# Performance work log

Hardware: AMD Instinct MI355X
Metric: run time of the kernel (lower is better)

The kernel has to match this reference:

```python
import jax, jax.numpy as jnp
import numpy as np

VOCAB, EMB, FEAT = 30000, 300, 2048
B, NQ, NW, NK = 256, 32, 12, 64


def setup_inputs() -> dict:
    key = jax.random.key(0)
    ks = jax.random.split(key, 10)
    return {
        "wv": jax.random.normal(ks[0], (VOCAB, EMB), jnp.float32),
        "Wf": jax.random.normal(ks[1], (EMB, FEAT), jnp.float32) * 0.02,
        "bf": jax.random.normal(ks[2], (EMB,), jnp.float32) * 0.02,
        "Wp": jax.random.normal(ks[3], (EMB, EMB), jnp.float32) * 0.05,
        "bp": jax.random.normal(ks[4], (EMB,), jnp.float32) * 0.02,
        "Wm": jax.random.normal(ks[5], (EMB, EMB), jnp.float32) * 0.05,
        "bm": jax.random.normal(ks[6], (EMB,), jnp.float32) * 0.02,
        "feature": jax.random.normal(ks[7], (B, NK, FEAT), jnp.float32),
        "query": jax.random.randint(ks[8], (B, NQ, NW), 0, VOCAB),
        "label": jax.random.randint(ks[9], (B, NK), 0, VOCAB),
    }


def reference(wv, Wf, bf, Wp, bp, Wm, bm, feature, query, label):
    # Dropouts act as identity in eval mode.
    eps = 1e-5
    q_emb = wv[query]                                   # [B, queries, words, D]
    k_emb = wv[label] + feature @ Wf.T + bf             # [B, objects, D]
    scale = 1.0 / np.sqrt(EMB)
    att = jnp.einsum('byqd,bkd->byqk', q_emb, k_emb) * scale
    att = jax.nn.softmax(att, axis=-1)                  # over objects
    q_max_att = jnp.max(att, axis=3)                    # [B, queries, words]
    neg_inf = -jnp.finfo(q_max_att.dtype).max
    q_max_att = jnp.where(query == 0, neg_inf, q_max_att)
    q_max_norm_att = jax.nn.softmax(q_max_att, axis=-1) / 5.0
    p_emb = jnp.einsum('byq,byqd->byd', q_max_norm_att, q_emb)  # [B, queries, D]
    p_emb = (p_emb @ Wp.T + bp) + eps * (p_emb @ Wm.T + bm)
    return p_emb, k_emb
```

## Files before the change

kernel.cpp:

```cpp
#include <hip/hip_runtime.h>

typedef unsigned short u16;
typedef unsigned int u32;
typedef __bf16 bf16x8 __attribute__((ext_vector_type(8)));
typedef float f32x4 __attribute__((ext_vector_type(4)));

#if defined(__has_builtin)
#  if __has_builtin(__builtin_amdgcn_cvt_pk_bf16_f32)
#    define PK_BF16 1
#  endif
#endif

__device__ __forceinline__ u16 f2bu(float f){
  u32 u = __float_as_uint(f);
  return (u16)((u + 0x7fffu + ((u >> 16) & 1u)) >> 16);
}
__device__ __forceinline__ float b2f(u16 u){
  union { float f; u32 i; } v; v.i = ((u32)u) << 16; return v.f;
}
__device__ __forceinline__ u32 pkbf(float a, float b){
#ifdef PK_BF16
  typedef __bf16 bf16x2 __attribute__((ext_vector_type(2)));
  union { bf16x2 h; u32 u; } c;
  c.h = __builtin_amdgcn_cvt_pk_bf16_f32(a, b);
  return c.u;
#else
  return (u32)f2bu(a) | ((u32)f2bu(b) << 16);
#endif
}
__device__ __forceinline__ void glds16(const u16* g, u16* l){
  __builtin_amdgcn_global_load_lds(
      (const __attribute__((address_space(1))) void*)g,
      (__attribute__((address_space(3))) void*)l, 16, 0, 0);
}
__device__ __forceinline__ void glds16f(const float* g, float* l){
  __builtin_amdgcn_global_load_lds(
      (const __attribute__((address_space(1))) void*)g,
      (__attribute__((address_space(3))) void*)l, 16, 0, 0);
}

__global__ __launch_bounds__(256) void prep_wc(
    const float* __restrict__ Wp, const float* __restrict__ bp,
    const float* __restrict__ Wm, const float* __restrict__ bm,
    u16* __restrict__ Wc, float* __restrict__ bc)
{
  int idx = blockIdx.x * 256 + threadIdx.x;
  if (idx < 384 * 160) {
    int n = idx / 160, k = (idx % 160) * 2;
    float v0 = 0.f, v1 = 0.f;
    if (n < 300 && k < 300) {
      v0 = Wp[n * 300 + k]     + 1e-5f * Wm[n * 300 + k];
      v1 = Wp[n * 300 + k + 1] + 1e-5f * Wm[n * 300 + k + 1];
    }
    ((u32*)Wc)[idx] = pkbf(v0, v1);
    if (idx < 384) bc[idx] = (idx < 300) ? bp[idx] + 1e-5f * bm[idx] : 0.f;
  }
}

__global__ __launch_bounds__(256) void prep_wv16(
    const float* __restrict__ wv, u16* __restrict__ wv16)
{
  int idx = blockIdx.x * 256 + threadIdx.x;
  if (idx < 30000 * 160) {
    int row = idx / 160, k = (idx % 160) * 2;
    float v0 = 0.f, v1 = 0.f;
    if (k < 300) {
      v0 = wv[(size_t)row * 300 + k];
      v1 = wv[(size_t)row * 300 + k + 1];
    }
    ((u32*)wv16)[idx] = pkbf(v0, v1);
  }
}

__global__ __launch_bounds__(256) void prep_wf16(
    const float* __restrict__ Wf, u16* __restrict__ Wf16)
{
  int i = blockIdx.x * 256 + threadIdx.x;
  if (i < 384 * 1024) {
    int row = i >> 10, c2 = (i & 1023) * 2;
    float v0 = 0.f, v1 = 0.f;
    if (row < 300) {
      v0 = Wf[(size_t)row * 2048 + c2];
      v1 = Wf[(size_t)row * 2048 + c2 + 1];
    }
    ((u32*)Wf16)[i] = pkbf(v0, v1);
  }
}

template <int GLDS>
__global__ __launch_bounds__(256) void gemm0_kernel(
    const float* __restrict__ A, const float* __restrict__ B,
    const u16* __restrict__ Af16, const u16* __restrict__ Bf16,
    const float* __restrict__ bias,
    const int* __restrict__ label, const float* __restrict__ wv,
    float* __restrict__ C, u16* __restrict__ kemb16)
{
  __shared__ __align__(16) u16 As[128 * 32];
  __shared__ __align__(16) u16 Bs[128 * 32];
  const int lda = 2048, K = 2048, nbn = 3, nsrc = 300;
  int t = threadIdx.x;
  int bm = (blockIdx.x / nbn) * 128;
  int bn = (blockIdx.x % nbn) * 128;
  int lane = t & 63, w = t >> 6;
  int wm = (w >> 1) * 64, wn = (w & 1) * 64;

  f32x4 acc[4][4];
  for (int i = 0; i < 4; i++)
    for (int j = 0; j < 4; j++)
      for (int r = 0; r < 4; r++) acc[i][j][r] = 0.f;

  int mrow = lane & 15, q = lane >> 4;

  for (int kk = 0; kk < K; kk += 32) {
    #pragma unroll
    for (int p = 0; p < 2; p++) {
      int idx = t + p * 256;
      int row = idx >> 2, ch = idx & 3;
      int brow = bn + row;
      if (brow >= nsrc) brow = 0;
      const float4* ap = (const float4*)&A[(size_t)(bm + row) * lda + kk + ch * 8];
      float4 a0 = ap[0], a1 = ap[1];
      const float4* bpp = (const float4*)&B[(size_t)brow * lda + kk + ch * 8];
      float4 b0 = bpp[0], b1 = bpp[1];
      union { u32 u[4]; uint4 v; } pa, pb;
      pa.u[0] = pkbf(a0.x, a0.y); pa.u[1] = pkbf(a0.z, a0.w);
      pa.u[2] = pkbf(a1.x, a1.y); pa.u[3] = pkbf(a1.z, a1.w);
      pb.u[0] = pkbf(b0.x, b0.y); pb.u[1] = pkbf(b0.z, b0.w);
      pb.u[2] = pkbf(b1.x, b1.y); pb.u[3] = pkbf(b1.z, b1.w);
      *(uint4*)&As[idx * 8] = pa.v;
      *(uint4*)&Bs[idx * 8] = pb.v;
    }
    __syncthreads();

    bf16x8 af[4], bfr[4];
    #pragma unroll
    for (int i = 0; i < 4; i++)
      af[i] = *(const bf16x8*)&As[(wm + i * 16 + mrow) * 32 + q * 8];
    #pragma unroll
    for (int j = 0; j < 4; j++)
      bfr[j] = *(const bf16x8*)&Bs[(wn + j * 16 + mrow) * 32 + q * 8];
    #pragma unroll
    for (int i = 0; i < 4; i++)
      #pragma unroll
      for (int j = 0; j < 4; j++)
        acc[i][j] = __builtin_amdgcn_mfma_f32_16x16x32_bf16(
            af[i], bfr[j], acc[i][j], 0, 0, 0);
    __syncthreads();
  }

  #pragma unroll
  for (int i = 0; i < 4; i++)
    #pragma unroll
    for (int j = 0; j < 4; j++) {
      int col = bn + wn + j * 16 + (lane & 15);
      int rb = bm + wm + i * 16 + (lane >> 4) * 4;
      #pragma unroll
      for (int r = 0; r < 4; r++) {
        int m = rb + r;
        if (col < 300) {
          float v = acc[i][j][r];
          v += bias[col] + wv[(size_t)label[m] * 300 + col];
          C[(size_t)m * 300 + col] = v;
          if (kemb16) kemb16[(size_t)m * 320 + col] = f2bu(v);
        } else if (kemb16 && col < 320) {
          kemb16[(size_t)m * 320 + col] = 0;
        }
      }
    }
}

__global__ __launch_bounds__(256) void gemm0v6_kernel(
    const float* __restrict__ A, const u16* __restrict__ Bf16,
    float* __restrict__ P3)
{
  __shared__ __align__(16) float As[128 * 32];
  __shared__ __align__(16) u16  Bs[128 * 32];
  int t = threadIdx.x;
  int lane = t & 63, w = t >> 6;
  int g = blockIdx.x;
  int xcd = g & 7, seq = g >> 3;
  int mloc = seq / 9, rem = seq % 9;
  int nn = rem % 3, kc = rem / 3;
  int bm = (xcd * 16 + mloc) * 128;
  int bn = nn * 128;
  int k0 = kc * 672, kend = (kc == 2) ? 2048 : k0 + 672;
  int wm = (w >> 1) * 64, wn = (w & 1) * 64;
  int mrow = lane & 15, q = lane >> 4;

  f32x4 acc[4][4];
  #pragma unroll
  for (int i = 0; i < 4; i++)
    #pragma unroll
    for (int j = 0; j < 4; j++)
      #pragma unroll
      for (int r = 0; r < 4; r++) acc[i][j][r] = 0.f;

  int rlA = lane >> 3, chA = lane & 7;
  int rlB = lane >> 2, chB = lane & 3;
  const float* gA = &A[(size_t)(bm + w * 32 + rlA) * 2048 + ((chA ^ rlA) << 2)];
  const u16*   gB = &Bf16[(size_t)(bn + w * 32 + rlB) * 2048 + (chB << 3)];
  float* lA = &As[(w * 32) * 32];
  u16*   lB = &Bs[(w * 32) * 32];

  for (int kk = k0; kk < kend; kk += 32) {
    #pragma unroll
    for (int p = 0; p < 4; p++)
      glds16f(gA + (size_t)p * 8 * 2048 + kk, lA + p * 8 * 32);
    #pragma unroll
    for (int p = 0; p < 2; p++)
      glds16(gB + (size_t)p * 16 * 2048 + kk, lB + p * 16 * 32);
    __syncthreads();

    bf16x8 af[4], bfr[4];
    #pragma unroll
    for (int i = 0; i < 4; i++) {
      int r = wm + i * 16 + mrow;
      int c0 = ((2 * q) ^ (r & 7)) * 4;
      int c1 = ((2 * q + 1) ^ (r & 7)) * 4;
      f32x4 x = *(const f32x4*)&As[r * 32 + c0];
      f32x4 y = *(const f32x4*)&As[r * 32 + c1];
      union { u32 u[4]; bf16x8 h; } cc;
      cc.u[0] = pkbf(x[0], x[1]); cc.u[1] = pkbf(x[2], x[3]);
      cc.u[2] = pkbf(y[0], y[1]); cc.u[3] = pkbf(y[2], y[3]);
      af[i] = cc.h;
    }
    #pragma unroll
    for (int j = 0; j < 4; j++)
      bfr[j] = *(const bf16x8*)&Bs[(wn + j * 16 + mrow) * 32 + q * 8];
    #pragma unroll
    for (int i = 0; i < 4; i++)
      #pragma unroll
      for (int j = 0; j < 4; j++)
        acc[i][j] = __builtin_amdgcn_mfma_f32_16x16x32_bf16(
            af[i], bfr[j], acc[i][j], 0, 0, 0);
    __syncthreads();
  }

  #pragma unroll
  for (int i = 0; i < 4; i++)
    #pragma unroll
    for (int j = 0; j < 4; j++) {
      int col = bn + wn + j * 16 + (lane & 15);
      if (col >= 300) continue;
      int rb = bm + wm + i * 16 + (lane >> 4) * 4;
      #pragma unroll
      for (int r = 0; r < 4; r++)
        P3[(size_t)kc * 4915200 + (size_t)(rb + r) * 300 + col] = acc[i][j][r];
    }
}

__global__ __launch_bounds__(256) void reduce_kernel(
    const float* __restrict__ P3, const float* __restrict__ bf,
    const int* __restrict__ label, const float* __restrict__ wv,
    float* __restrict__ C, u16* __restrict__ kemb16)
{
  int idx = blockIdx.x * 256 + threadIdx.x;
  if (idx >= 16384 * 80) return;
  int m = idx / 80, c4 = idx % 80;
  if (c4 < 75) {
    int c = c4 * 4;
    float4 a = *(const float4*)&P3[(size_t)m * 300 + c];
    float4 b = *(const float4*)&P3[(size_t)4915200 + (size_t)m * 300 + c];
    float4 d = *(const float4*)&P3[(size_t)9830400 + (size_t)m * 300 + c];
    float4 wvv = *(const float4*)&wv[(size_t)label[m] * 300 + c];
    float4 bfv = *(const float4*)&bf[c];
    float4 v;
    v.x = a.x + b.x + d.x + bfv.x + wvv.x;
    v.y = a.y + b.y + d.y + bfv.y + wvv.y;
    v.z = a.z + b.z + d.z + bfv.z + wvv.z;
    v.w = a.w + b.w + d.w + bfv.w + wvv.w;
    *(float4*)&C[(size_t)m * 300 + c] = v;
    union { u16 h[4]; uint2 u; } o;
    o.h[0] = f2bu(v.x); o.h[1] = f2bu(v.y);
    o.h[2] = f2bu(v.z); o.h[3] = f2bu(v.w);
    *(uint2*)&kemb16[(size_t)m * 320 + c] = o.u;
  } else {
    int c = 300 + (c4 - 75) * 4;
    uint2 z; z.x = 0; z.y = 0;
    *(uint2*)&kemb16[(size_t)m * 320 + c] = z;
  }
}

#define KES 344
template <int FULL>
__global__ __launch_bounds__(256) void attn_kernel(
    const float* __restrict__ wv, const u16* __restrict__ wv16,
    const int* __restrict__ query,
    const float* __restrict__ kout, const u16* __restrict__ kemb16,
    u16* __restrict__ praw)
{
  __shared__ __align__(16) u16 ke[64 * KES];
  __shared__ __align__(16) int qoff[192];
  __shared__ __align__(16) float awd[192];
  __shared__ __align__(16) float wt[192];

  int blk = blockIdx.x, b = blk >> 1, bh = blk & 1;
  int t = threadIdx.x;
  int lane = t & 63, w = t >> 6;

  if (FULL) {
    for (int i = t; i < 2560; i += 256) {
      int row = i / 40, ch = i % 40;
      *(uint4*)&ke[row * KES + ch * 8] =
          *(const uint4*)&kemb16[(size_t)(b * 64 + row) * 320 + ch * 8];
    }
  } else {
    for (int i = t; i < 4800; i += 256) {
      int row = i / 75, c4 = i % 75;
      float4 v = *(const float4*)&kout[(size_t)(b * 64 + row) * 300 + c4 * 4];
      *(u32*)&ke[row * KES + c4 * 4]     = pkbf(v.x, v.y);
      *(u32*)&ke[row * KES + c4 * 4 + 2] = pkbf(v.z, v.w);
    }
    for (int i = t; i < 640; i += 256) {
      int row = i / 10, c2 = i % 10;
      *(u32*)&ke[row * KES + 300 + c2 * 2] = 0;
    }
  }
  if (t < 192)
    qoff[t] = query[b * 384 + bh * 192 + t] * (FULL ? 320 : 300);
  __syncthreads();

  int mrow = lane & 15, q = lane >> 4;
  f32x4 acc[3][4];
  #pragma unroll
  for (int i = 0; i < 3; i++)
    #pragma unroll
    for (int j = 0; j < 4; j++)
      #pragma unroll
      for (int r = 0; r < 4; r++) acc[i][j][r] = 0.f;

  int base[3];
  #pragma unroll
  for (int i = 0; i < 3; i++) base[i] = qoff[w * 48 + i * 16 + mrow];
  int keb = mrow * KES + q * 8;

  bf16x8 afn[3];
  #pragma unroll
  for (int i = 0; i < 3; i++) {
    if (FULL)
      afn[i] = *(const bf16x8*)&wv16[(size_t)base[i] + q * 8];
  }

  for (int k0 = 0; k0 < 320; k0 += 32) {
    bf16x8 af[3], bfr[4];
    #pragma unroll
    for (int i = 0; i < 3; i++) {
      if (FULL) {
        af[i] = afn[i];
        if (k0 + 32 < 320)
          afn[i] = *(const bf16x8*)&wv16[(size_t)base[i] + k0 + 32 + q * 8];
      } else {
        int cs = k0 + q * 8;
        union { u32 u[4]; bf16x8 h; } c;
        if (cs + 8 <= 300) {
          const float4* p = (const float4*)&wv[(size_t)base[i] + cs];
          float4 x = p[0], y = p[1];
          c.u[0] = pkbf(x.x, x.y); c.u[1] = pkbf(x.z, x.w);
          c.u[2] = pkbf(y.x, y.y); c.u[3] = pkbf(y.z, y.w);
        } else if (cs < 300) {
          float4 x = *(const float4*)&wv[(size_t)base[i] + 296];
          c.u[0] = pkbf(x.x, x.y); c.u[1] = pkbf(x.z, x.w);
          c.u[2] = 0; c.u[3] = 0;
        } else {
          c.u[0] = 0; c.u[1] = 0; c.u[2] = 0; c.u[3] = 0;
        }
        af[i] = c.h;
      }
    }
    #pragma unroll
    for (int j = 0; j < 4; j++)
      bfr[j] = *(const bf16x8*)&ke[j * 16 * KES + keb + k0];
    #pragma unroll
    for (int i = 0; i < 3; i++)
      #pragma unroll
      for (int j = 0; j < 4; j++)
        acc[i][j] = __builtin_amdgcn_mfma_f32_16x16x32_bf16(
            af[i], bfr[j], acc[i][j], 0, 0, 0);
  }

  const float scale = 0.05773502691896258f;
  #pragma unroll
  for (int i = 0; i < 3; i++)
    #pragma unroll
    for (int r = 0; r < 4; r++) {
      float mx = fmaxf(fmaxf(acc[i][0][r], acc[i][1][r]),
                       fmaxf(acc[i][2][r], acc[i][3][r]));
      #pragma unroll
      for (int d = 1; d < 16; d <<= 1)
        mx = fmaxf(mx, __shfl_xor(mx, d));
      float se = 0.f;
      #pragma unroll
      for (int j = 0; j < 4; j++)
        se += __expf((acc[i][j][r] - mx) * scale);
      #pragma unroll
      for (int d = 1; d < 16; d <<= 1)
        se += __shfl_xor(se, d);
      if (mrow == 0) {
        int wl = w * 48 + i * 16 + q * 4 + r;
        awd[wl] = (qoff[wl] == 0) ? -3.402823466e38f : (1.0f / se);
      }
    }
  __syncthreads();

  if (t < 16) {
    int yb = t * 12;
    float m2 = -3.402823466e38f;
    for (int i = 0; i < 12; i++) m2 = fmaxf(m2, awd[yb + i]);
    float e[12], s2 = 0.f;
    for (int i = 0; i < 12; i++) { e[i] = __expf(awd[yb + i] - m2); s2 += e[i]; }
    float inv = 0.2f / s2;
    for (int i = 0; i < 12; i++) wt[yb + i] = e[i] * inv;
  }
  __syncthreads();

  #pragma unroll
  for (int yy = 0; yy < 4; yy++) {
    int yl = w * 4 + yy;
    int row = b * 32 + bh * 16 + yl;
    if (FULL) {
      if (lane < 40) {
        float s[8];
        #pragma unroll
        for (int e = 0; e < 8; e++) s[e] = 0.f;
        for (int i = 0; i < 12; i++) {
          float g = wt[yl * 12 + i];
          union { uint4 v; u16 h[8]; } qv;
          qv.v = *(const uint4*)&wv16[(size_t)qoff[yl * 12 + i] + lane * 8];
          #pragma unroll
          for (int e = 0; e < 8; e++) s[e] += g * b2f(qv.h[e]);
        }
        union { uint4 v; u16 h[8]; } o;
        #pragma unroll
        for (int e = 0; e < 8; e++) o.h[e] = f2bu(s[e]);
        *(uint4*)&praw[(size_t)row * 320 + lane * 8] = o.v;
      }
    } else {
      #pragma unroll
      for (int c = 0; c < 5; c++) {
        int d = c * 64 + lane;
        float s = 0.f;
        if (d < 300)
          for (int i = 0; i < 12; i++)
            s += wt[yl * 12 + i] * wv[(size_t)qoff[yl * 12 + i] + d];
        praw[(size_t)row * 320 + d] = f2bu(s);
      }
    }
  }
}

__global__ __launch_bounds__(256) void proj_kernel(
    const u16* __restrict__ praw, const u16* __restrict__ Wc,
    const float* __restrict__ bc, float* __restrict__ P)
{
  __shared__ __align__(16) u16 As[128 * 32];
  __shared__ __align__(16) u16 Bs[128 * 32];
  int t = threadIdx.x;
  int bm = (blockIdx.x / 3) * 128;
  int bn = (blockIdx.x % 3) * 128;
  int lane = t & 63, w = t >> 6;
  int wm = (w >> 1) * 64, wn = (w & 1) * 64;

  f32x4 acc[4][4];
  for (int i = 0; i < 4; i++)
    for (int j = 0; j < 4; j++)
      for (int r = 0; r < 4; r++) acc[i][j][r] = 0.f;

  int mrow = lane & 15, q = lane >> 4;

  for (int kk = 0; kk < 320; kk += 32) {
    int r0 = w * 32;
    int rl = lane >> 2, ch = lane & 3;
    #pragma unroll
    for (int p = 0; p < 2; p++) {
      int row = r0 + p * 16 + rl;
      glds16(&praw[(size_t)(bm + row) * 320 + kk + ch * 8],
             &As[(r0 + p * 16) * 32]);
      glds16(&Wc[(size_t)(bn + row) * 320 + kk + ch * 8],
             &Bs[(r0 + p * 16) * 32]);
    }
    __syncthreads();

    bf16x8 af[4], bfr[4];
    #pragma unroll
    for (int i = 0; i < 4; i++)
      af[i] = *(const bf16x8*)&As[(wm + i * 16 + mrow) * 32 + q * 8];
    #pragma unroll
    for (int j = 0; j < 4; j++)
      bfr[j] = *(const bf16x8*)&Bs[(wn + j * 16 + mrow) * 32 + q * 8];
    #pragma unroll
    for (int i = 0; i < 4; i++)
      #pragma unroll
      for (int j = 0; j < 4; j++)
        acc[i][j] = __builtin_amdgcn_mfma_f32_16x16x32_bf16(
            af[i], bfr[j], acc[i][j], 0, 0, 0);
    __syncthreads();
  }

  #pragma unroll
  for (int i = 0; i < 4; i++)
    #pragma unroll
    for (int j = 0; j < 4; j++) {
      int col = bn + wn + j * 16 + (lane & 15);
      if (col >= 300) continue;
      int rb = bm + wm + i * 16 + (lane >> 4) * 4;
      #pragma unroll
      for (int r = 0; r < 4; r++)
        P[(size_t)(rb + r) * 300 + col] = acc[i][j][r] + bc[col];
    }
}

extern "C" void kernel_launch(void* const* d_in, const int* in_sizes, int n_in,
                              void* d_out, int out_size, void* d_ws,
                              size_t ws_size, hipStream_t stream)
{
  const float* wv      = (const float*)d_in[0];
  const float* Wf      = (const float*)d_in[1];
  const float* bf      = (const float*)d_in[2];
  const float* Wp      = (const float*)d_in[3];
  const float* bp      = (const float*)d_in[4];
  const float* Wm      = (const float*)d_in[5];
  const float* bm      = (const float*)d_in[6];
  const float* feature = (const float*)d_in[7];
  const int*   query   = (const int*)d_in[8];
  const int*   label   = (const int*)d_in[9];

  float* out   = (float*)d_out;
  float* p_out = out;
  float* k_out = out + 2457600;

  char* ws = (char*)d_ws;
  int t2 = ws_size >= (size_t)103857664;
  int t1 = ws_size >= (size_t)35175936;
  u16 *wf16 = 0, *wv16 = 0, *kemb16 = 0, *praw, *Wc;
  float* bc;
  float* P3 = (float*)ws;
  if (t2) {
    wv16   = (u16*)(ws + 67108864);
    kemb16 = (u16*)(ws + 86308864);
    praw   = (u16*)(ws + 96794624);
    Wc     = (u16*)(ws + 102037504);
    wf16   = (u16*)(ws + 102283264);
    bc     = (float*)(ws + 103856128);
  } else if (t1) {
    wv16   = (u16*)ws;
    kemb16 = (u16*)(ws + 19200000);
    praw   = (u16*)(ws + 29685760);
    Wc     = (u16*)(ws + 34928640);
    bc     = (float*)(ws + 35174400);
  } else {
    praw   = (u16*)ws;
    Wc     = (u16*)(ws + 5242880);
    bc     = (float*)(ws + 5488640);
  }

  prep_wc<<<240, 256, 0, stream>>>(Wp, bp, Wm, bm, Wc, bc);
  if (t1 || t2)
    prep_wv16<<<18750, 256, 0, stream>>>(wv, wv16);
  if (t2) {
    prep_wf16<<<1536, 256, 0, stream>>>(Wf, wf16);
    gemm0v6_kernel<<<1152, 256, 0, stream>>>(feature, wf16, P3);
    reduce_kernel<<<5120, 256, 0, stream>>>(P3, bf, label, wv,
                                            k_out, kemb16);
  } else {
    gemm0_kernel<0><<<384, 256, 0, stream>>>(feature, Wf, 0, 0, bf,
                                             label, wv, k_out, kemb16);
  }

  if (t1 || t2)
    attn_kernel<1><<<512, 256, 0, stream>>>(wv, wv16, query, k_out,
                                            kemb16, praw);
  else
    attn_kernel<0><<<512, 256, 0, stream>>>(wv, wv16, query, k_out,
                                            kemb16, praw);

  proj_kernel<<<192, 256, 0, stream>>>(praw, Wc, bc, p_out);
}
```

Before: 369.0 us.

## Restructure feature GEMM into independent per-wave 64x64 tiles without block barriers

The block-cooperative 128x128 GEMM is replaced with per-wave 64x64 output tiles. Each wave stages its own A slice in a private LDS region and loads bf16 B fragments straight from global memory into registers, prefetching the next step. This removes __syncthreads and B shared-memory staging. In exchange, A rows are re-fetched by six N-tiles instead of three, and A reads use a single LDS buffer with little latency hiding.

New measurement: 380.3 us. +3.1%, slower.

```diff
diff --git a/kernel.cpp b/kernel.cpp
--- a/kernel.cpp
+++ b/kernel.cpp
@@ -169,22 +169,18 @@
     }
 }
 
-__global__ __launch_bounds__(256) void gemm0v6_kernel(
+__global__ __launch_bounds__(256) void gemm0v7_kernel(
     const float* __restrict__ A, const u16* __restrict__ Bf16,
     float* __restrict__ P3)
 {
-  __shared__ __align__(16) float As[128 * 32];
-  __shared__ __align__(16) u16  Bs[128 * 32];
+  __shared__ __align__(16) float As[4][64 * 32];
   int t = threadIdx.x;
   int lane = t & 63, w = t >> 6;
-  int g = blockIdx.x;
-  int xcd = g & 7, seq = g >> 3;
-  int mloc = seq / 9, rem = seq % 9;
-  int nn = rem % 3, kc = rem / 3;
-  int bm = (xcd * 16 + mloc) * 128;
-  int bn = nn * 128;
-  int k0 = kc * 672, kend = (kc == 2) ? 2048 : k0 + 672;
-  int wm = (w >> 1) * 64, wn = (w & 1) * 64;
+  int u = blockIdx.x * 4 + w;
+  int kc = u / 1536, rem = u % 1536;
+  int bm = (rem / 6) * 64, bn = (rem % 6) * 64;
+  int k0 = (kc == 0) ? 0 : ((kc == 1) ? 704 : 1376);
+  int nit = (kc == 0) ? 22 : 21;
   int mrow = lane & 15, q = lane >> 4;
 
   f32x4 acc[4][4];
@@ -196,53 +192,64 @@
       for (int r = 0; r < 4; r++) acc[i][j][r] = 0.f;
 
   int rlA = lane >> 3, chA = lane & 7;
-  int rlB = lane >> 2, chB = lane & 3;
-  const float* gA = &A[(size_t)(bm + w * 32 + rlA) * 2048 + ((chA ^ rlA) << 2)];
-  const u16*   gB = &Bf16[(size_t)(bn + w * 32 + rlB) * 2048 + (chB << 3)];
-  float* lA = &As[(w * 32) * 32];
-  u16*   lB = &Bs[(w * 32) * 32];
-
-  for (int kk = k0; kk < kend; kk += 32) {
-    #pragma unroll
-    for (int p = 0; p < 4; p++)
-      glds16f(gA + (size_t)p * 8 * 2048 + kk, lA + p * 8 * 32);
-    #pragma unroll
-    for (int p = 0; p < 2; p++)
-      glds16(gB + (size_t)p * 16 * 2048 + kk, lB + p * 16 * 32);
-    __syncthreads();
-
-    bf16x8 af[4], bfr[4];
+  const float* gA = &A[(size_t)(bm + rlA) * 2048 + ((chA ^ rlA) << 2) + k0];
+  float* lA = As[w];
+
+  const u16* pB[4];
+  #pragma unroll
+  for (int j = 0; j < 4; j++)
+    pB[j] = &Bf16[(size_t)(bn + j * 16 + mrow) * 2048 + q * 8 + k0];
+
+  #pragma unroll
+  for (int p = 0; p < 8; p++)
+    glds16f(gA + (size_t)p * 8 * 2048, lA + p * 8 * 32);
+  bf16x8 bc[4];
+  #pragma unroll
+  for (int j = 0; j < 4; j++) bc[j] = *(const bf16x8*)(pB[j]);
+
+  for (int it = 0; it < nit; ++it) {
+    int kk = it * 32;
+    bf16x8 af[4];
     #pragma unroll
     for (int i = 0; i < 4; i++) {
-      int r = wm + i * 16 + mrow;
+      int r = i * 16 + mrow;
       int c0 = ((2 * q) ^ (r & 7)) * 4;
       int c1 = ((2 * q + 1) ^ (r & 7)) * 4;
-      f32x4 x = *(const f32x4*)&As[r * 32 + c0];
-      f32x4 y = *(const f32x4*)&As[r * 32 + c1];
+      f32x4 x = *(const f32x4*)&lA[r * 32 + c0];
+      f32x4 y = *(const f32x4*)&lA[r * 32 + c1];
       union { u32 u[4]; bf16x8 h; } cc;
       cc.u[0] = pkbf(x[0], x[1]); cc.u[1] = pkbf(x[2], x[3]);
       cc.u[2] = pkbf(y[0], y[1]); cc.u[3] = pkbf(y[2], y[3]);
       af[i] = cc.h;
     }
-    #pragma unroll
-    for (int j = 0; j < 4; j++)
-      bfr[j] = *(const bf16x8*)&Bs[(wn + j * 16 + mrow) * 32 + q * 8];
+    bf16x8 bnx[4];
+    if (it + 1 < nit) {
+      #pragma unroll
+      for (int j = 0; j < 4; j++)
+        bnx[j] = *(const bf16x8*)(pB[j] + kk + 32);
+    }
     #pragma unroll
     for (int i = 0; i < 4; i++)
       #pragma unroll
       for (int j = 0; j < 4; j++)
         acc[i][j] = __builtin_amdgcn_mfma_f32_16x16x32_bf16(
-            af[i], bfr[j], acc[i][j], 0, 0, 0);
-    __syncthreads();
+            af[i], bc[j], acc[i][j], 0, 0, 0);
+    if (it + 1 < nit) {
+      #pragma unroll
+      for (int p = 0; p < 8; p++)
+        glds16f(gA + (size_t)p * 8 * 2048 + kk + 32, lA + p * 8 * 32);
+      #pragma unroll
+      for (int j = 0; j < 4; j++) bc[j] = bnx[j];
+    }
   }
 
   #pragma unroll
   for (int i = 0; i < 4; i++)
     #pragma unroll
     for (int j = 0; j < 4; j++) {
-      int col = bn + wn + j * 16 + (lane & 15);
+      int col = bn + j * 16 + (lane & 15);
       if (col >= 300) continue;
-      int rb = bm + wm + i * 16 + (lane >> 4) * 4;
+      int rb = bm + i * 16 + (lane >> 4) * 4;
       #pragma unroll
       for (int r = 0; r < 4; r++)
         P3[(size_t)kc * 4915200 + (size_t)(rb + r) * 300 + col] = acc[i][j][r];
@@ -558,7 +565,7 @@
     prep_wv16<<<18750, 256, 0, stream>>>(wv, wv16);
   if (t2) {
     prep_wf16<<<1536, 256, 0, stream>>>(Wf, wf16);
-    gemm0v6_kernel<<<1152, 256, 0, stream>>>(feature, wf16, P3);
+    gemm0v7_kernel<<<1152, 256, 0, stream>>>(feature, wf16, P3);
     reduce_kernel<<<5120, 256, 0, stream>>>(P3, bf, label, wv,
                                             k_out, kemb16);
   } else {
```
